# Kernel optimization log

Hardware: AMD Instinct MI355X
Metric: run time of the kernel (lower is better)

Reference implementation:

```python
import jax, jax.numpy as jnp
import numpy as np

N_HEAD = 16

def setup_inputs() -> dict:
    key = jax.random.key(0)
    ks = jax.random.split(key, 7)
    B, T, C = 2, 2048, 1024
    return {
        "query": jax.random.normal(ks[0], (B, T, C), jnp.float32),
        "key": jax.random.normal(ks[1], (B, T, C), jnp.float32),
        "value": jax.random.normal(ks[2], (B, T, C), jnp.float32),
        "Wq": jax.random.normal(ks[3], (C, C), jnp.float32) * (1.0 / np.sqrt(C)),
        "Wk": jax.random.normal(ks[4], (C, C), jnp.float32) * (1.0 / np.sqrt(C)),
        "Wv": jax.random.normal(ks[5], (C, C), jnp.float32) * (1.0 / np.sqrt(C)),
        "Wo": jax.random.normal(ks[6], (C, C), jnp.float32) * (1.0 / np.sqrt(C)),
    }

def reference(query, key, value, Wq, Wk, Wv, Wo):
    B, T, C = query.shape
    H = N_HEAD
    D = C // H
    # QKV projections (torch Linear: x @ W.T, no bias)
    q = (query @ Wq.T).reshape(B, T, H, D).transpose(0, 2, 1, 3)  # [B,H,T,D]
    k = (key   @ Wk.T).reshape(B, T, H, D).transpose(0, 2, 1, 3)
    v = (value @ Wv.T).reshape(B, T, H, D).transpose(0, 2, 1, 3)
    scale = 1.0 / np.sqrt(D).astype(np.float32)
    att = jnp.einsum("bhqd,bhkd->bhqk", q, k) * scale  # [B,H,T,T]
    att = jax.nn.softmax(att, axis=-1)
    y = jnp.einsum("bhqk,bhkd->bhqd", att, v)  # [B,H,T,D]
    y = y.transpose(0, 2, 1, 3).reshape(B, T, C)
    return y @ Wo.T
```

## Files before the change

### kernel.cpp

```cpp
#include <hip/hip_runtime.h>
#include <hip/hip_bf16.h>
#include <cstdint>

typedef __attribute__((ext_vector_type(8))) short bf16x8;
typedef __attribute__((ext_vector_type(4))) float f32x4;
typedef __attribute__((ext_vector_type(16))) float f32x16;
typedef __attribute__((ext_vector_type(4))) unsigned short us4;

#define MFMA16(a, b, c) __builtin_amdgcn_mfma_f32_16x16x32_bf16((a), (b), (c), 0, 0, 0)
#define MFMA32(a, b, c) __builtin_amdgcn_mfma_f32_32x32x16_bf16((a), (b), (c), 0, 0, 0)
#define GLB_PTR(p) ((const __attribute__((address_space(1))) void*)(p))
#define LDS_PTR(p) ((__attribute__((address_space(3))) void*)(p))

__device__ __forceinline__ unsigned short f2bf(float f) {
    union { float f; unsigned u; } v; v.f = f;
    unsigned r = v.u + 0x7fffu + ((v.u >> 16) & 1u);
    return (unsigned short)(r >> 16);
}

__device__ __forceinline__ unsigned cvtpk(float lo, float hi) {
    unsigned r;
    asm("v_cvt_pk_bf16_f32 %0, %1, %2" : "=v"(r) : "v"(lo), "v"(hi));
    return r;
}

struct CastArgs {
    const float* src[7];
    unsigned short* dst[7];
    int n4[7];
};

__global__ __launch_bounds__(256) void cast_f32_bf16(CastArgs a) {
    const int id = blockIdx.y;
    const float4* s = (const float4*)a.src[id];
    us4* d = (us4*)a.dst[id];
    const int n4 = a.n4[id];
    for (int i = blockIdx.x * blockDim.x + threadIdx.x; i < n4;
         i += gridDim.x * blockDim.x) {
        float4 v = s[i];
        us4 o;
        o.x = f2bf(v.x); o.y = f2bf(v.y); o.z = f2bf(v.z); o.w = f2bf(v.w);
        d[i] = o;
    }
}

struct GemmGroup {
    const unsigned short* A[3];
    const unsigned short* B[3];
    unsigned short* C[3];
};

__global__ __launch_bounds__(256, 2)
void gemm_qkv(GemmGroup gg, int M, int N, int K) {
    __shared__ __align__(16) unsigned short As[2][128 * 32];
    __shared__ __align__(16) unsigned short Bs[2][128 * 32];
    const int z = blockIdx.z;
    const unsigned short* __restrict__ A = gg.A[z];
    const unsigned short* __restrict__ B = gg.B[z];
    unsigned short* __restrict__ C = gg.C[z];
    const int t = threadIdx.x;
    const int lane = t & 63, wave = t >> 6;
    const int row0 = blockIdx.x * 128, col0 = blockIdx.y * 128;
    const int wr = (wave >> 1) * 64, wc = (wave & 1) * 64;
    const int r = lane & 15, g = lane >> 4;
    const int srow = t >> 2;
    const int scol = (t & 3) * 8;

#define GSTAGE(buf, k0)                                                        \
    {                                                                          \
        _Pragma("unroll")                                                      \
        for (int i = 0; i < 2; ++i) {                                          \
            const int rr = i * 64 + srow;                                      \
            __builtin_amdgcn_global_load_lds(                                  \
                GLB_PTR(A + (size_t)(row0 + rr) * K + (k0) + scol),            \
                LDS_PTR(&As[buf][rr * 32 + scol]), 16, 0, 0);                  \
            __builtin_amdgcn_global_load_lds(                                  \
                GLB_PTR(B + (size_t)(col0 + rr) * K + (k0) + scol),            \
                LDS_PTR(&Bs[buf][rr * 32 + scol]), 16, 0, 0);                  \
        }                                                                      \
    }

    f32x4 acc[4][4] = {};
    GSTAGE(0, 0);
    __syncthreads();

    for (int it = 0; it < 32; ++it) {
        const int buf = it & 1;
        if (it + 1 < 32) GSTAGE(buf ^ 1, (it + 1) * 32);
        bf16x8 a[4], b[4];
#pragma unroll
        for (int m = 0; m < 4; ++m)
            a[m] = *(const bf16x8*)(&As[buf][(wr + m * 16 + r) * 32 + g * 8]);
#pragma unroll
        for (int n = 0; n < 4; ++n)
            b[n] = *(const bf16x8*)(&Bs[buf][(wc + n * 16 + r) * 32 + g * 8]);
        __builtin_amdgcn_s_setprio(1);
#pragma unroll
        for (int m = 0; m < 4; ++m)
#pragma unroll
            for (int n = 0; n < 4; ++n)
                acc[m][n] = MFMA16(a[m], b[n], acc[m][n]);
        __builtin_amdgcn_s_setprio(0);
        __syncthreads();
    }
#undef GSTAGE

    const float sc = (z == 0) ? 0.18033688011112042f : 1.0f;
#pragma unroll
    for (int m = 0; m < 4; ++m) {
#pragma unroll
        for (int n = 0; n < 4; ++n) {
#pragma unroll
            for (int i = 0; i < 4; ++i) {
                const int row = row0 + wr + m * 16 + g * 4 + i;
                const int col = col0 + wc + n * 16 + r;
                const int b_ = row >> 11, tt = row & 2047;
                const int h = col >> 6, d = col & 63;
                const int bh = b_ * 16 + h;
                size_t idx;
                if (z == 2) {
                    const int l = (d & 31) + 32 * ((tt >> 3) & 1);
                    idx = ((((size_t)(bh * 32 + (tt >> 6))) * 2 + (d >> 5)) * 4 +
                           ((tt >> 4) & 3)) * 512 + l * 8 + (tt & 7);
                } else {
                    const int l = (tt & 31) + 32 * ((d >> 3) & 1);
                    idx = (((size_t)(bh * 64 + (tt >> 5))) * 4 + (d >> 4)) * 512 +
                          l * 8 + (d & 7);
                }
                C[idx] = f2bf(acc[m][n][i] * sc);
            }
        }
    }
}

__global__ __launch_bounds__(256, 2)
void gemm_wo(const unsigned short* __restrict__ A,
             const unsigned short* __restrict__ B,
             float* __restrict__ C, int M, int N, int K) {
    __shared__ __align__(16) unsigned short As[2][64 * 32];
    __shared__ __align__(16) unsigned short Bs[2][128 * 32];
    const int t = threadIdx.x;
    const int lane = t & 63, wave = t >> 6;
    const int row0 = blockIdx.x * 64, col0 = blockIdx.y * 128;
    const int wc = wave * 32;
    const int r = lane & 15, g = lane >> 4;
    const int srow = t >> 2;
    const int scol = (t & 3) * 8;

#define WSTAGE(buf, k0)                                                        \
    {                                                                          \
        __builtin_amdgcn_global_load_lds(                                      \
            GLB_PTR(A + (size_t)(row0 + srow) * K + (k0) + scol),              \
            LDS_PTR(&As[buf][srow * 32 + scol]), 16, 0, 0);                    \
        _Pragma("unroll")                                                      \
        for (int i = 0; i < 2; ++i) {                                          \
            const int rr = i * 64 + srow;                                      \
            __builtin_amdgcn_global_load_lds(                                  \
                GLB_PTR(B + (size_t)(col0 + rr) * K + (k0) + scol),            \
                LDS_PTR(&Bs[buf][rr * 32 + scol]), 16, 0, 0);                  \
        }                                                                      \
    }

    f32x4 acc[4][2] = {};
    WSTAGE(0, 0);
    __syncthreads();

    for (int it = 0; it < 32; ++it) {
        const int buf = it & 1;
        if (it + 1 < 32) WSTAGE(buf ^ 1, (it + 1) * 32);
        bf16x8 a[4], b[2];
#pragma unroll
        for (int m = 0; m < 4; ++m)
            a[m] = *(const bf16x8*)(&As[buf][(m * 16 + r) * 32 + g * 8]);
#pragma unroll
        for (int n = 0; n < 2; ++n)
            b[n] = *(const bf16x8*)(&Bs[buf][(wc + n * 16 + r) * 32 + g * 8]);
        __builtin_amdgcn_s_setprio(1);
#pragma unroll
        for (int m = 0; m < 4; ++m)
#pragma unroll
            for (int n = 0; n < 2; ++n)
                acc[m][n] = MFMA16(a[m], b[n], acc[m][n]);
        __builtin_amdgcn_s_setprio(0);
        __syncthreads();
    }
#undef WSTAGE

#pragma unroll
    for (int m = 0; m < 4; ++m)
#pragma unroll
        for (int n = 0; n < 2; ++n)
#pragma unroll
            for (int i = 0; i < 4; ++i) {
                const int row = row0 + m * 16 + g * 4 + i;
                const int col = col0 + wc + n * 16 + r;
                C[(size_t)row * N + col] = acc[m][n][i];
            }
}

__global__ __launch_bounds__(128, 2)
void attn_fwd(const unsigned short* __restrict__ Qpk,
              const unsigned short* __restrict__ Kpk,
              const unsigned short* __restrict__ Vpk,
              unsigned short* __restrict__ Y) {
    __shared__ __align__(16) unsigned short kv_lds[2][16][512];
    const int t = threadIdx.x, lane = t & 63, w = t >> 6;
    const int q31 = lane & 31, hi = lane >> 5;

    const int flat = blockIdx.x;
    const int swz = (flat & 7) * 128 + (flat >> 3);
    const int qt = swz & 31, bh = swz >> 5;
    const int qb0 = qt * 64;

    const unsigned short* Qb = Qpk + ((size_t)(bh * 64 + qt * 2 + w)) * 2048;
    const unsigned short* Kb = Kpk + (size_t)bh * 131072;
    const unsigned short* Vb = Vpk + (size_t)bh * 131072;

    bf16x8 qf[4];
#pragma unroll
    for (int s = 0; s < 4; ++s)
        qf[s] = *(const bf16x8*)(Qb + s * 512 + lane * 8);

    f32x16 o0 = {}, o1 = {};
    float l_ = 0.f;

#define STAGE(buf, kv0)                                                        \
    {                                                                          \
        _Pragma("unroll")                                                      \
        for (int i = 0; i < 8; ++i) {                                          \
            const int f = w * 8 + i;                                           \
            const unsigned short* src =                                        \
                (f < 8 ? Kb : Vb) + (kv0) * 64 + (f & 7) * 512 + lane * 8;     \
            __builtin_amdgcn_global_load_lds(                                  \
                GLB_PTR(src), LDS_PTR(&kv_lds[buf][f][lane * 8]), 16, 0, 0);   \
        }                                                                      \
    }

    STAGE(0, 0);
    __syncthreads();

    for (int it = 0; it < 32; ++it) {
        const int buf = it & 1;
        if (it + 1 < 32) STAGE(buf ^ 1, (it + 1) * 64);

        bf16x8 kf[8];
#pragma unroll
        for (int i = 0; i < 8; ++i)
            kf[i] = *(const bf16x8*)(&kv_lds[buf][i][lane * 8]);
        f32x16 s0, s1;
#pragma unroll
        for (int r = 0; r < 16; ++r) { s0[r] = -12.f; s1[r] = -12.f; }
        __builtin_amdgcn_s_setprio(1);
#pragma unroll
        for (int s = 0; s < 4; ++s) s0 = MFMA32(kf[s], qf[s], s0);
#pragma unroll
        for (int s = 0; s < 4; ++s) s1 = MFMA32(kf[4 + s], qf[s], s1);
        __builtin_amdgcn_s_setprio(0);

        float p[32];
#pragma unroll
        for (int r = 0; r < 16; ++r) p[r] = __builtin_amdgcn_exp2f(s0[r]);
#pragma unroll
        for (int r = 0; r < 16; ++r) p[16 + r] = __builtin_amdgcn_exp2f(s1[r]);

        float sm[16];
#pragma unroll
        for (int r = 0; r < 16; ++r) sm[r] = p[r] + p[16 + r];
#pragma unroll
        for (int d = 8; d > 0; d >>= 1)
#pragma unroll
            for (int r = 0; r < d; ++r) sm[r] += sm[r + d];
        l_ += sm[0] + __shfl_xor(sm[0], 32);

        unsigned c[16];
#pragma unroll
        for (int i = 0; i < 16; ++i) c[i] = cvtpk(p[2 * i], p[2 * i + 1]);

        bf16x8 vf[8];
#pragma unroll
        for (int i = 0; i < 8; ++i)
            vf[i] = *(const bf16x8*)(&kv_lds[buf][8 + i][lane * 8]);

        __builtin_amdgcn_s_setprio(1);
#pragma unroll
        for (int s = 0; s < 4; ++s) {
            const int base = (s >> 1) * 8 + (s & 1) * 4;
            unsigned a0 = c[base + 0], b0 = c[base + 2];
            unsigned a1 = c[base + 1], b1 = c[base + 3];
            asm volatile("v_permlane32_swap_b32 %0, %1" : "+v"(a0), "+v"(b0));
            asm volatile("v_permlane32_swap_b32 %0, %1" : "+v"(a1), "+v"(b1));
            union { unsigned u[4]; bf16x8 v; } pb;
            pb.u[0] = a0; pb.u[1] = a1; pb.u[2] = b0; pb.u[3] = b1;
            o0 = MFMA32(vf[s], pb.v, o0);
            o1 = MFMA32(vf[4 + s], pb.v, o1);
        }
        __builtin_amdgcn_s_setprio(0);

        __syncthreads();
    }
#undef STAGE

    unsigned short (*yb)[68] = (unsigned short (*)[68])kv_lds;
    const float rinv = 1.0f / l_;
#pragma unroll
    for (int r = 0; r < 16; ++r) {
        const int dd = (r & 3) + 8 * (r >> 2) + 4 * hi;
        yb[w * 32 + q31][dd] = f2bf(o0[r] * rinv);
        yb[w * 32 + q31][32 + dd] = f2bf(o1[r] * rinv);
    }
    __syncthreads();
    const int b_ = bh >> 4, h = bh & 15;
#pragma unroll
    for (int i = 0; i < 8; ++i) {
        const int row = i * 8 + (t >> 4);
        const int col = (t & 15) * 4;
        *(us4*)(Y + ((size_t)(b_ * 2048 + qb0 + row)) * 1024 + h * 64 + col) =
            *(const us4*)(&yb[row][col]);
    }
}

extern "C" void kernel_launch(void* const* d_in, const int* in_sizes, int n_in,
                              void* d_out, int out_size, void* d_ws, size_t ws_size,
                              hipStream_t stream) {
    uint8_t* ws = (uint8_t*)d_ws;
    unsigned short* xq = (unsigned short*)(ws + 0);
    unsigned short* xk = (unsigned short*)(ws + 8388608);
    unsigned short* xv = (unsigned short*)(ws + 16777216);
    unsigned short* wq = (unsigned short*)(ws + 25165824);
    unsigned short* wk = (unsigned short*)(ws + 27262976);
    unsigned short* wv = (unsigned short*)(ws + 29360128);
    unsigned short* wo = (unsigned short*)(ws + 31457280);
    unsigned short* Qp = (unsigned short*)(ws + 33554432);
    unsigned short* Kp = (unsigned short*)(ws + 41943040);
    unsigned short* Vp = (unsigned short*)(ws + 50331648);
    unsigned short* y  = xq;

    CastArgs ca;
    ca.src[0] = (const float*)d_in[0]; ca.dst[0] = xq; ca.n4[0] = 4194304 / 4;
    ca.src[1] = (const float*)d_in[1]; ca.dst[1] = xk; ca.n4[1] = 4194304 / 4;
    ca.src[2] = (const float*)d_in[2]; ca.dst[2] = xv; ca.n4[2] = 4194304 / 4;
    ca.src[3] = (const float*)d_in[3]; ca.dst[3] = wq; ca.n4[3] = 1048576 / 4;
    ca.src[4] = (const float*)d_in[4]; ca.dst[4] = wk; ca.n4[4] = 1048576 / 4;
    ca.src[5] = (const float*)d_in[5]; ca.dst[5] = wv; ca.n4[5] = 1048576 / 4;
    ca.src[6] = (const float*)d_in[6]; ca.dst[6] = wo; ca.n4[6] = 1048576 / 4;
    cast_f32_bf16<<<dim3(512, 7), 256, 0, stream>>>(ca);

    GemmGroup gg;
    gg.A[0] = xq; gg.B[0] = wq; gg.C[0] = Qp;
    gg.A[1] = xk; gg.B[1] = wk; gg.C[1] = Kp;
    gg.A[2] = xv; gg.B[2] = wv; gg.C[2] = Vp;
    gemm_qkv<<<dim3(32, 8, 3), 256, 0, stream>>>(gg, 4096, 1024, 1024);

    attn_fwd<<<dim3(1024), 128, 0, stream>>>(Qp, Kp, Vp, y);

    gemm_wo<<<dim3(64, 8), 256, 0, stream>>>(y, wo, (float*)d_out, 4096, 1024, 1024);
}
```

Measured before the change: 132.7 us.

## Deepen LDS pipelines with vmcnt waits and enlarge attention tiles

Both GEMMs move from double to triple buffering. They prefetch two stages ahead, replace the full __syncthreads with an explicit vmcnt wait plus s_barrier, and drop the trailing barrier. The attention kernel now uses 4 waves per block covering 128 query rows with a 4-slot KV ring prefetched three stages ahead, which halves the grid. The aim is to hide global-load latency and cut barrier stalls, at the cost of more LDS per block, which may lower occupancy.

```diff
diff --git a/kernel.cpp b/kernel.cpp
--- a/kernel.cpp
+++ b/kernel.cpp
@@ -11,6 +11,7 @@
 #define MFMA32(a, b, c) __builtin_amdgcn_mfma_f32_32x32x16_bf16((a), (b), (c), 0, 0, 0)
 #define GLB_PTR(p) ((const __attribute__((address_space(1))) void*)(p))
 #define LDS_PTR(p) ((__attribute__((address_space(3))) void*)(p))
+#define WAITV(n) asm volatile("s_waitcnt vmcnt(" #n ")" ::: "memory")
 
 __device__ __forceinline__ unsigned short f2bf(float f) {
     union { float f; unsigned u; } v; v.f = f;
@@ -52,8 +53,8 @@
 
 __global__ __launch_bounds__(256, 2)
 void gemm_qkv(GemmGroup gg, int M, int N, int K) {
-    __shared__ __align__(16) unsigned short As[2][128 * 32];
-    __shared__ __align__(16) unsigned short Bs[2][128 * 32];
+    __shared__ __align__(16) unsigned short As[3][128 * 32];
+    __shared__ __align__(16) unsigned short Bs[3][128 * 32];
     const int z = blockIdx.z;
     const unsigned short* __restrict__ A = gg.A[z];
     const unsigned short* __restrict__ B = gg.B[z];
@@ -66,34 +67,37 @@
     const int srow = t >> 2;
     const int scol = (t & 3) * 8;
 
-#define GSTAGE(buf, k0)                                                        \
+#define GSTAGE(sl, k0)                                                         \
     {                                                                          \
         _Pragma("unroll")                                                      \
         for (int i = 0; i < 2; ++i) {                                          \
             const int rr = i * 64 + srow;                                      \
             __builtin_amdgcn_global_load_lds(                                  \
                 GLB_PTR(A + (size_t)(row0 + rr) * K + (k0) + scol),            \
-                LDS_PTR(&As[buf][rr * 32 + scol]), 16, 0, 0);                  \
+                LDS_PTR(&As[sl][rr * 32 + scol]), 16, 0, 0);                   \
             __builtin_amdgcn_global_load_lds(                                  \
                 GLB_PTR(B + (size_t)(col0 + rr) * K + (k0) + scol),            \
-                LDS_PTR(&Bs[buf][rr * 32 + scol]), 16, 0, 0);                  \
+                LDS_PTR(&Bs[sl][rr * 32 + scol]), 16, 0, 0);                   \
         }                                                                      \
     }
 
     f32x4 acc[4][4] = {};
     GSTAGE(0, 0);
-    __syncthreads();
+    GSTAGE(1, 32);
 
     for (int it = 0; it < 32; ++it) {
-        const int buf = it & 1;
-        if (it + 1 < 32) GSTAGE(buf ^ 1, (it + 1) * 32);
+        if (it < 31) WAITV(4); else WAITV(0);
+        __builtin_amdgcn_s_barrier();
+        __builtin_amdgcn_sched_barrier(0);
+        if (it + 2 < 32) GSTAGE((it + 2) % 3, (it + 2) * 32);
+        const int sl = it % 3;
         bf16x8 a[4], b[4];
 #pragma unroll
         for (int m = 0; m < 4; ++m)
-            a[m] = *(const bf16x8*)(&As[buf][(wr + m * 16 + r) * 32 + g * 8]);
+            a[m] = *(const bf16x8*)(&As[sl][(wr + m * 16 + r) * 32 + g * 8]);
 #pragma unroll
         for (int n = 0; n < 4; ++n)
-            b[n] = *(const bf16x8*)(&Bs[buf][(wc + n * 16 + r) * 32 + g * 8]);
+            b[n] = *(const bf16x8*)(&Bs[sl][(wc + n * 16 + r) * 32 + g * 8]);
         __builtin_amdgcn_s_setprio(1);
 #pragma unroll
         for (int m = 0; m < 4; ++m)
@@ -101,7 +105,6 @@
             for (int n = 0; n < 4; ++n)
                 acc[m][n] = MFMA16(a[m], b[n], acc[m][n]);
         __builtin_amdgcn_s_setprio(0);
-        __syncthreads();
     }
 #undef GSTAGE
 
@@ -137,8 +140,8 @@
 void gemm_wo(const unsigned short* __restrict__ A,
              const unsigned short* __restrict__ B,
              float* __restrict__ C, int M, int N, int K) {
-    __shared__ __align__(16) unsigned short As[2][64 * 32];
-    __shared__ __align__(16) unsigned short Bs[2][128 * 32];
+    __shared__ __align__(16) unsigned short As[3][64 * 32];
+    __shared__ __align__(16) unsigned short Bs[3][128 * 32];
     const int t = threadIdx.x;
     const int lane = t & 63, wave = t >> 6;
     const int row0 = blockIdx.x * 64, col0 = blockIdx.y * 128;
@@ -147,34 +150,37 @@
     const int srow = t >> 2;
     const int scol = (t & 3) * 8;
 
-#define WSTAGE(buf, k0)                                                        \
+#define WSTAGE(sl, k0)                                                         \
     {                                                                          \
         __builtin_amdgcn_global_load_lds(                                      \
             GLB_PTR(A + (size_t)(row0 + srow) * K + (k0) + scol),              \
-            LDS_PTR(&As[buf][srow * 32 + scol]), 16, 0, 0);                    \
+            LDS_PTR(&As[sl][srow * 32 + scol]), 16, 0, 0);                     \
         _Pragma("unroll")                                                      \
         for (int i = 0; i < 2; ++i) {                                          \
             const int rr = i * 64 + srow;                                      \
             __builtin_amdgcn_global_load_lds(                                  \
                 GLB_PTR(B + (size_t)(col0 + rr) * K + (k0) + scol),            \
-                LDS_PTR(&Bs[buf][rr * 32 + scol]), 16, 0, 0);                  \
+                LDS_PTR(&Bs[sl][rr * 32 + scol]), 16, 0, 0);                   \
         }                                                                      \
     }
 
     f32x4 acc[4][2] = {};
     WSTAGE(0, 0);
-    __syncthreads();
+    WSTAGE(1, 32);
 
     for (int it = 0; it < 32; ++it) {
-        const int buf = it & 1;
-        if (it + 1 < 32) WSTAGE(buf ^ 1, (it + 1) * 32);
+        if (it < 31) WAITV(3); else WAITV(0);
+        __builtin_amdgcn_s_barrier();
+        __builtin_amdgcn_sched_barrier(0);
+        if (it + 2 < 32) WSTAGE((it + 2) % 3, (it + 2) * 32);
+        const int sl = it % 3;
         bf16x8 a[4], b[2];
 #pragma unroll
         for (int m = 0; m < 4; ++m)
-            a[m] = *(const bf16x8*)(&As[buf][(m * 16 + r) * 32 + g * 8]);
+            a[m] = *(const bf16x8*)(&As[sl][(m * 16 + r) * 32 + g * 8]);
 #pragma unroll
         for (int n = 0; n < 2; ++n)
-            b[n] = *(const bf16x8*)(&Bs[buf][(wc + n * 16 + r) * 32 + g * 8]);
+            b[n] = *(const bf16x8*)(&Bs[sl][(wc + n * 16 + r) * 32 + g * 8]);
         __builtin_amdgcn_s_setprio(1);
 #pragma unroll
         for (int m = 0; m < 4; ++m)
@@ -182,7 +188,6 @@
             for (int n = 0; n < 2; ++n)
                 acc[m][n] = MFMA16(a[m], b[n], acc[m][n]);
         __builtin_amdgcn_s_setprio(0);
-        __syncthreads();
     }
 #undef WSTAGE
 
@@ -198,21 +203,21 @@
             }
 }
 
-__global__ __launch_bounds__(128, 2)
+__global__ __launch_bounds__(256, 2)
 void attn_fwd(const unsigned short* __restrict__ Qpk,
               const unsigned short* __restrict__ Kpk,
               const unsigned short* __restrict__ Vpk,
               unsigned short* __restrict__ Y) {
-    __shared__ __align__(16) unsigned short kv_lds[2][16][512];
+    __shared__ __align__(16) unsigned short kv_lds[4][16][512];
     const int t = threadIdx.x, lane = t & 63, w = t >> 6;
     const int q31 = lane & 31, hi = lane >> 5;
 
     const int flat = blockIdx.x;
-    const int swz = (flat & 7) * 128 + (flat >> 3);
-    const int qt = swz & 31, bh = swz >> 5;
-    const int qb0 = qt * 64;
-
-    const unsigned short* Qb = Qpk + ((size_t)(bh * 64 + qt * 2 + w)) * 2048;
+    const int swz = (flat & 7) * 64 + (flat >> 3);
+    const int qt = swz & 15, bh = swz >> 4;
+    const int qb0 = qt * 128;
+
+    const unsigned short* Qb = Qpk + ((size_t)(bh * 64 + qt * 4 + w)) * 2048;
     const unsigned short* Kb = Kpk + (size_t)bh * 131072;
     const unsigned short* Vb = Vpk + (size_t)bh * 131072;
 
@@ -220,33 +225,40 @@
 #pragma unroll
     for (int s = 0; s < 4; ++s)
         qf[s] = *(const bf16x8*)(Qb + s * 512 + lane * 8);
+    WAITV(0);
 
     f32x16 o0 = {}, o1 = {};
     float l_ = 0.f;
 
-#define STAGE(buf, kv0)                                                        \
+#define STAGE(sl, kv0)                                                         \
     {                                                                          \
         _Pragma("unroll")                                                      \
-        for (int i = 0; i < 8; ++i) {                                          \
-            const int f = w * 8 + i;                                           \
+        for (int i = 0; i < 4; ++i) {                                          \
+            const int f = w * 4 + i;                                           \
             const unsigned short* src =                                        \
                 (f < 8 ? Kb : Vb) + (kv0) * 64 + (f & 7) * 512 + lane * 8;     \
             __builtin_amdgcn_global_load_lds(                                  \
-                GLB_PTR(src), LDS_PTR(&kv_lds[buf][f][lane * 8]), 16, 0, 0);   \
+                GLB_PTR(src), LDS_PTR(&kv_lds[sl][f][lane * 8]), 16, 0, 0);    \
         }                                                                      \
     }
 
     STAGE(0, 0);
-    __syncthreads();
+    STAGE(1, 64);
+    STAGE(2, 128);
 
     for (int it = 0; it < 32; ++it) {
-        const int buf = it & 1;
-        if (it + 1 < 32) STAGE(buf ^ 1, (it + 1) * 64);
+        if (it < 30) WAITV(8);
+        else if (it == 30) WAITV(4);
+        else WAITV(0);
+        __builtin_amdgcn_s_barrier();
+        __builtin_amdgcn_sched_barrier(0);
+        if (it + 3 < 32) STAGE((it + 3) & 3, (it + 3) * 64);
+        const int sl = it & 3;
 
         bf16x8 kf[8];
 #pragma unroll
         for (int i = 0; i < 8; ++i)
-            kf[i] = *(const bf16x8*)(&kv_lds[buf][i][lane * 8]);
+            kf[i] = *(const bf16x8*)(&kv_lds[sl][i][lane * 8]);
         f32x16 s0, s1;
 #pragma unroll
         for (int r = 0; r < 16; ++r) { s0[r] = -12.f; s1[r] = -12.f; }
@@ -279,7 +291,7 @@
         bf16x8 vf[8];
 #pragma unroll
         for (int i = 0; i < 8; ++i)
-            vf[i] = *(const bf16x8*)(&kv_lds[buf][8 + i][lane * 8]);
+            vf[i] = *(const bf16x8*)(&kv_lds[sl][8 + i][lane * 8]);
 
         __builtin_amdgcn_s_setprio(1);
 #pragma unroll
@@ -295,10 +307,10 @@
             o1 = MFMA32(vf[4 + s], pb.v, o1);
         }
         __builtin_amdgcn_s_setprio(0);
-
-        __syncthreads();
     }
 #undef STAGE
+
+    __syncthreads();
 
     unsigned short (*yb)[68] = (unsigned short (*)[68])kv_lds;
     const float rinv = 1.0f / l_;
@@ -312,7 +324,7 @@
     const int b_ = bh >> 4, h = bh & 15;
 #pragma unroll
     for (int i = 0; i < 8; ++i) {
-        const int row = i * 8 + (t >> 4);
+        const int row = i * 16 + (t >> 4);
         const int col = (t & 15) * 4;
         *(us4*)(Y + ((size_t)(b_ * 2048 + qb0 + row)) * 1024 + h * 64 + col) =
             *(const us4*)(&yb[row][col]);
@@ -351,7 +363,7 @@
     gg.A[2] = xv; gg.B[2] = wv; gg.C[2] = Vp;
     gemm_qkv<<<dim3(32, 8, 3), 256, 0, stream>>>(gg, 4096, 1024, 1024);
 
-    attn_fwd<<<dim3(1024), 128, 0, stream>>>(Qp, Kp, Vp, y);
+    attn_fwd<<<dim3(512), 256, 0, stream>>>(Qp, Kp, Vp, y);
 
     gemm_wo<<<dim3(64, 8), 256, 0, stream>>>(y, wo, (float*)d_out, 4096, 1024, 1024);
 }
```

Result: faster. 123.8 us (-6.7%).
